# Performance work log

Hardware: AMD Instinct MI355X
Metric: run time of the kernel (lower is better)

The kernel has to match this reference:

```python
import jax, jax.numpy as jnp
import numpy as np
import math

N = 32768
C = 128
K = 16
CHUNK = 2048
LN_EPS = float(C)  # original code calls torch.nn.LayerNorm(C, C): second positional arg is eps -> eps = 128.0 (faithful)


def knn_idx(coords):
    """Brute-force KNN on full coords [N,4] (matches knn_points(x_C, x_C, K=16)), chunked over queries."""
    def one_chunk(q):  # q: [CHUNK,4]
        d = jnp.sum((q[:, None, :] - coords[None, :, :]) ** 2, axis=-1)  # [CHUNK,N]
        return jax.lax.top_k(-d, K)[1]  # ascending distance (return_sorted=True)
    qs = coords.reshape(-1, CHUNK, coords.shape[-1])
    return jax.lax.map(one_chunk, qs).reshape(-1, K)  # [N,K]


def layer_norm(x, g, b):
    mu = jnp.mean(x, axis=-1, keepdims=True)
    var = jnp.mean((x - mu) ** 2, axis=-1, keepdims=True)
    return (x - mu) / jnp.sqrt(var + LN_EPS) * g + b


def self_attention(x_f, xyz_enc, new_feature, qw, qb, kw, kb, vw, vb):
    Q = x_f @ qw + qb                              # [N,C]
    nf = new_feature + xyz_enc                     # [N,K,C]
    Kt = nf @ kw + kb                              # [N,K,C]
    scores = jnp.einsum('nkd,nd->nk', Kt, Q) / math.sqrt(C)
    a = jax.nn.softmax(scores, axis=-1)            # [N,K]
    V = nf @ vw + vb                               # [N,K,C]
    return jnp.einsum('nk,nkd->nd', a, V)          # [N,C]


def setup_inputs() -> dict:
    key = jax.random.key(0)
    ks = jax.random.split(key, 22)
    xyz = jax.random.uniform(ks[0], (N, 3), dtype=jnp.float32) * 100.0
    coords = jnp.concatenate([jnp.zeros((N, 1), jnp.float32), xyz], axis=1)  # [N,4] batch col = 0
    feats = jax.random.normal(ks[1], (N, C), dtype=jnp.float32)
    s = 0.02
    def lin(k, din, dout):
        kw, kb = jax.random.split(k)
        return jax.random.normal(kw, (din, dout), jnp.float32) * s, jax.random.normal(kb, (dout,), jnp.float32) * s
    pos_w, pos_b = lin(ks[2], 3, C)
    pos1_w, pos1_b = lin(ks[3], 3, C)
    qw0, qb0 = lin(ks[4], C, C); kw0, kb0 = lin(ks[5], C, C); vw0, vb0 = lin(ks[6], C, C)
    qw1, qb1 = lin(ks[7], C, C); kw1, kb1 = lin(ks[8], C, C); vw1, vb1 = lin(ks[9], C, C)
    lin_w, lin_b = lin(ks[10], C, C)  # MinkowskiConvolution kernel_size=1 == pointwise linear
    return {
        'coords': coords, 'feats': feats,
        'pos_w': pos_w, 'pos_b': pos_b, 'pos1_w': pos1_w, 'pos1_b': pos1_b,
        'qw0': qw0, 'qb0': qb0, 'kw0': kw0, 'kb0': kb0, 'vw0': vw0, 'vb0': vb0,
        'qw1': qw1, 'qb1': qb1, 'kw1': kw1, 'kb1': kb1, 'vw1': vw1, 'vb1': vb1,
        'lin_w': lin_w, 'lin_b': lin_b,
        'g0': jnp.ones((C,), jnp.float32), 'be0': jnp.zeros((C,), jnp.float32),
        'g1': jnp.ones((C,), jnp.float32), 'be1': jnp.zeros((C,), jnp.float32),
    }


def reference(coords, feats, pos_w, pos_b, pos1_w, pos1_b,
              qw0, qb0, kw0, kb0, vw0, vb0,
              qw1, qb1, kw1, kb1, vw1, vb1,
              lin_w, lin_b, g0, be0, g1, be1):
    idx = knn_idx(coords)                           # [N,K]
    xyz = coords[:, 1:]                             # [N,3]
    new_xyz = xyz[:, None, :] - xyz[idx]            # [N,K,3] relative offsets
    # block 1
    xyz_enc = new_xyz @ pos_w + pos_b               # [N,K,C]
    nf = feats[idx]                                 # gather [N,K,C]
    o = self_attention(feats, xyz_enc, nf, qw0, qb0, kw0, kb0, vw0, vb0)
    # block 2: re-gather updated features with same idx
    nf1 = o[idx]
    xyz_enc1 = new_xyz @ pos1_w + pos1_b
    o = self_attention(o, xyz_enc1, nf1, qw1, qb1, kw1, kb1, vw1, vb1)
    # residual + LN, pointwise conv, residual + LN
    h = layer_norm(feats + o, g0, be0)
    h1 = h @ lin_w + lin_b
    return layer_norm(h + h1, g1, be1)
```

## Files before the change

### kernel.cpp

```cpp
#include <hip/hip_runtime.h>
#include <stdint.h>

#define NPT 32768

typedef unsigned int u32;
typedef unsigned short u16;
typedef unsigned long long u64;

typedef short v8s __attribute__((ext_vector_type(8)));
typedef float v4f __attribute__((ext_vector_type(4)));

__device__ __forceinline__ float b2f(u16 u) {
  union { u32 u; float f; } x; x.u = ((u32)u) << 16; return x.f;
}
__device__ __forceinline__ u16 f2b(float f) {
  union { float f; u32 u; } x; x.f = f;
  u32 u = x.u;
  return (u16)((u + 0x7fffu + ((u >> 16) & 1u)) >> 16);
}
__device__ __forceinline__ bool probe_f32(const void* coords) {
  return ((const u16*)coords)[1] == 0;
}
__device__ __forceinline__ float ldany(const void* p, long i, bool f32) {
  return f32 ? ((const float*)p)[i] : b2f(((const u16*)p)[i]);
}
__device__ __forceinline__ float wsum(float v) {
#pragma unroll
  for (int m = 1; m < 64; m <<= 1) v += __shfl_xor(v, m, 64);
  return v;
}

#define GC 16
#define GH 6.25f
#define GINV 0.16f
#define NCELL (GC * GC * GC)

__device__ __forceinline__ int cell1d(float v) {
  int c = (int)(v * GINV);
  return c > (GC - 1) ? (GC - 1) : (c < 0 ? 0 : c);
}

__global__ __launch_bounds__(256) void conv_coords_hist(const void* __restrict__ coords,
                                                        float* __restrict__ cx, float* __restrict__ cy,
                                                        float* __restrict__ cz, int* __restrict__ cellStart,
                                                        int* __restrict__ pcell) {
  const bool f32 = probe_f32(coords);
  int i = blockIdx.x * 256 + threadIdx.x;
  float x = ldany(coords, (long)i * 4 + 1, f32);
  float y = ldany(coords, (long)i * 4 + 2, f32);
  float z = ldany(coords, (long)i * 4 + 3, f32);
  cx[i] = x; cy[i] = y; cz[i] = z;
  int c = (cell1d(z) * GC + cell1d(y)) * GC + cell1d(x);
  pcell[i] = c;
  atomicAdd(&cellStart[c + 1], 1);
}

__global__ __launch_bounds__(256) void conv_featsS(const void* __restrict__ coords,
                                                   const void* __restrict__ feats,
                                                   const float4* __restrict__ sortedP,
                                                   u16* __restrict__ featsS) {
  const bool f32 = probe_f32(coords);
  long i = (long)blockIdx.x * 256 + threadIdx.x;
  int s = (int)(i >> 7), c = (int)(i & 127);
  long orig = (long)__float_as_int(sortedP[s].w);
  featsS[i] = f32 ? f2b(((const float*)feats)[orig * 128 + c]) : ((const u16*)feats)[orig * 128 + c];
}

__global__ __launch_bounds__(256) void grid_scan(int* __restrict__ cellStart, int* __restrict__ cellPtr) {
  __shared__ int part[256];
  const int t = threadIdx.x;
  int local[16]; int s = 0;
#pragma unroll
  for (int i = 0; i < 16; i++) { local[i] = cellStart[1 + t * 16 + i]; s += local[i]; }
  part[t] = s;
  __syncthreads();
  for (int off = 1; off < 256; off <<= 1) {
    int v = (t >= off) ? part[t - off] : 0;
    __syncthreads();
    part[t] += v;
    __syncthreads();
  }
  int run = (t == 0) ? 0 : part[t - 1];
#pragma unroll
  for (int i = 0; i < 16; i++) {
    int c = t * 16 + i;
    cellPtr[c] = run;
    run += local[i];
    cellStart[c + 1] = run;
  }
}

__global__ __launch_bounds__(256) void grid_scatter(const float* __restrict__ cx, const float* __restrict__ cy,
                                                    const float* __restrict__ cz, const int* __restrict__ pcell,
                                                    int* __restrict__ cellPtr, float4* __restrict__ sortedP,
                                                    int* __restrict__ rank) {
  int i = blockIdx.x * 256 + threadIdx.x;
  int c = pcell[i];
  int pos = atomicAdd(&cellPtr[c], 1);
  sortedP[pos] = make_float4(cx[i], cy[i], cz[i], __int_as_float(i));
  rank[i] = pos;
}

__global__ __launch_bounds__(256) void knn_grid(const float4* __restrict__ sortedP,
                                                const int* __restrict__ cellStart,
                                                const int* __restrict__ rank,
                                                u16* __restrict__ idxout) {
  const int lane = threadIdx.x & 63;
  const int gl = lane & 15;
  const int grp = lane >> 4;
  const int q = blockIdx.x * 16 + (threadIdx.x >> 4);
  const float4 p = sortedP[q];
  const float qx = p.x, qy = p.y, qz = p.z;
  const int qcx = cell1d(qx), qcy = cell1d(qy), qcz = cell1d(qz);

  u64 R = ~0ull;

  auto key_of = [&](int g) -> u64 {
    float4 sp = sortedP[g];
    float dx = __fsub_rn(qx, sp.x), dy = __fsub_rn(qy, sp.y), dzc = __fsub_rn(qz, sp.z);
    float d = __fadd_rn(__fadd_rn(__fmul_rn(dx, dx), __fmul_rn(dy, dy)), __fmul_rn(dzc, dzc));
    return ((u64)__float_as_uint(d) << 32) | (u32)__float_as_int(sp.w);
  };

  auto shfl64 = [&](u64 v, int s) -> u64 {
    int lo = __shfl((int)(u32)v, s, 16);
    int hi = __shfl((int)(u32)(v >> 32), s, 16);
    return ((u64)(u32)hi << 32) | (u32)lo;
  };
  auto sxg = [&](u64 v, int m) -> u64 {
    int lo = __shfl_xor((int)(u32)v, m, 64);
    int hi = __shfl_xor((int)(u32)(v >> 32), m, 64);
    return ((u64)(u32)hi << 32) | (u32)lo;
  };
  auto upg = [&](u64 v) -> u64 {
    int lo = __shfl_up((int)(u32)v, 1, 16);
    int hi = __shfl_up((int)(u32)(v >> 32), 1, 16);
    return ((u64)(u32)hi << 32) | (u32)lo;
  };

  auto insert_one = [&](u64 kk) {
    u64 prev = upg(R);
    if (gl == 0) prev = 0ull;
    R = (kk < R) ? ((kk >= prev) ? kk : prev) : R;
  };

  auto batch_merge = [&](u64 key) {
    u64 k15 = shfl64(R, 15);
    u64 mask = __ballot(key < k15);
    u32 mymask = (u32)((mask >> (grp * 16)) & 0xffffu);
    if (mymask == 0) return;
    int pcount = __popc(mymask);
    if (pcount <= 8) {
      u32 mm = mymask;
      while (mm) {
        int s = __ffs((int)mm) - 1;
        mm &= mm - 1;
        insert_one(shfl64(key, s));
      }
      return;
    }
#pragma unroll
    for (int k = 2; k <= 16; k <<= 1) {
#pragma unroll
      for (int j = k >> 1; j > 0; j >>= 1) {
        u64 o = sxg(key, j);
        bool up = ((gl & k) == 0);
        bool lower = ((gl & j) == 0);
        u64 mn = key < o ? key : o;
        u64 mx = key < o ? o : key;
        key = (lower == up) ? mn : mx;
      }
    }
    u64 s = sxg(key, 15);
    u64 mn = R < s ? R : s;
#pragma unroll
    for (int j = 8; j > 0; j >>= 1) {
      u64 o = sxg(mn, j);
      bool lower = ((gl & j) == 0);
      u64 lo = mn < o ? mn : o;
      u64 hi = mn < o ? o : mn;
      mn = lower ? lo : hi;
    }
    R = mn;
  };

  auto scan_range_grp = [&](int s0, int s1) {
    for (int base = s0; base < s1; base += 16) {
      int g = base + gl;
      u64 key = (g < s1) ? key_of(g) : ~0ull;
      batch_merge(key);
    }
  };

  {
    const int rord[9] = { 4, 1, 3, 5, 7, 0, 2, 6, 8 };
    int rs[9], rl[9];
#pragma unroll
    for (int s_ = 0; s_ < 9; s_++) {
      int row = rord[s_];
      int dz = row / 3 - 1, dy = row % 3 - 1;
      int z = qcz + dz, y = qcy + dy;
      if (z < 0 || z > GC - 1 || y < 0 || y > GC - 1) { rs[s_] = 0; rl[s_] = 0; }
      else {
        int rb = (z * GC + y) * GC;
        int xlo = qcx - 1 < 0 ? 0 : qcx - 1;
        int xhi = qcx + 1 > GC - 1 ? GC - 1 : qcx + 1;
        int s = cellStart[rb + xlo], e = cellStart[rb + xhi + 1];
        rs[s_] = s; rl[s_] = e - s;
      }
    }
    int cum[10]; cum[0] = 0;
#pragma unroll
    for (int i = 0; i < 9; i++) cum[i + 1] = cum[i] + rl[i];
    int total = cum[9];
    for (int base = 0; base < total; base += 16) {
      int pp = base + gl;
      u64 key = ~0ull;
      if (pp < total) {
        int g = 0;
#pragma unroll
        for (int i = 0; i < 9; i++) {
          if (pp >= cum[i] && pp < cum[i + 1]) g = rs[i] + (pp - cum[i]);
        }
        key = key_of(g);
      }
      batch_merge(key);
    }
  }

  {
    u64 k15 = shfl64(R, 15);
    float d15 = __uint_as_float((u32)(k15 >> 32));
    float b1 = GH * 1.0f;
    if (!(d15 < b1 * b1 * 0.998f)) {
      for (int r = 2; r < GC; ++r) {
        int zlo = qcz - r < 0 ? 0 : qcz - r, zhi = qcz + r > GC - 1 ? GC - 1 : qcz + r;
        for (int z = zlo; z <= zhi; ++z) {
          int adz = z - qcz; adz = adz < 0 ? -adz : adz;
          bool ez = (adz == r);
          int ylo = qcy - r < 0 ? 0 : qcy - r, yhi = qcy + r > GC - 1 ? GC - 1 : qcy + r;
          for (int y = ylo; y <= yhi; ++y) {
            int ady = y - qcy; ady = ady < 0 ? -ady : ady;
            bool ey = (ady == r);
            int rb = (z * GC + y) * GC;
            if (ez || ey) {
              int xlo = qcx - r < 0 ? 0 : qcx - r, xhi = qcx + r > GC - 1 ? GC - 1 : qcx + r;
              scan_range_grp(cellStart[rb + xlo], cellStart[rb + xhi + 1]);
            } else {
              int xm = qcx - r, xp = qcx + r;
              if (xm >= 0) scan_range_grp(cellStart[rb + xm], cellStart[rb + xm + 1]);
              if (xp <= GC - 1) scan_range_grp(cellStart[rb + xp], cellStart[rb + xp + 1]);
            }
          }
        }
        k15 = shfl64(R, 15);
        d15 = __uint_as_float((u32)(k15 >> 32));
        float bound = GH * (float)r;
        if (d15 < bound * bound * 0.998f) break;
      }
    }
  }

  idxout[(size_t)q * 16 + gl] = (u16)rank[(int)(u32)R];
}

__global__ __launch_bounds__(256) void prep_tables(
    const void* coords,
    const void* pw0, const void* pb0, const void* kw0, const void* kb0, const void* vw0, const void* vb0,
    const void* pw1, const void* pb1, const void* kw1, const void* kb1, const void* vw1, const void* vb1,
    float* __restrict__ tbl, int* __restrict__ cellStart) {
  const bool f32 = probe_f32(coords);
  const int tid = blockIdx.x * 256 + threadIdx.x;
  if (tid <= NCELL) cellStart[tid] = 0;
  const int lane = threadIdx.x & 63;
  const int o = blockIdx.x * 4 + (threadIdx.x >> 6);
  const int l = o >> 10;
  const int rem = o & 1023;
  const void* PW = l ? pw1 : pw0;
  const void* PB = l ? pb1 : pb0;
  const void* KW = l ? kw1 : kw0;
  const void* KB = l ? kb1 : kb0;
  const void* VW = l ? vw1 : vw0;
  const void* VB = l ? vb1 : vb0;
  float acc, extra = 0.f;
  if (rem < 768) {
    bool isV = rem >= 384;
    int r2 = isV ? rem - 384 : rem;
    int i = r2 >> 7, c = r2 & 127;
    const void* W = isV ? VW : KW;
    acc = ldany(PW, i * 128 + lane, f32) * ldany(W, (long)lane * 128 + c, f32)
        + ldany(PW, i * 128 + lane + 64, f32) * ldany(W, (long)(lane + 64) * 128 + c, f32);
  } else {
    bool isV = rem >= 896;
    int c = rem & 127;
    const void* W = isV ? VW : KW;
    const void* B = isV ? VB : KB;
    acc = ldany(PB, lane, f32) * ldany(W, (long)lane * 128 + c, f32)
        + ldany(PB, lane + 64, f32) * ldany(W, (long)(lane + 64) * 128 + c, f32);
    extra = ldany(B, c, f32);
  }
  acc = wsum(acc) + extra;
  if (lane == 0) tbl[l * 1024 + rem] = acc;
}

__global__ __launch_bounds__(256) void prep_bfrag_all(const void* __restrict__ coords,
                                                      const void* __restrict__ qw0, const void* __restrict__ kw0,
                                                      const void* __restrict__ vw0, const void* __restrict__ qw1,
                                                      const void* __restrict__ kw1, const void* __restrict__ vw1,
                                                      const void* __restrict__ linw, u16* __restrict__ Bf0,
                                                      u16* __restrict__ Bf1, u16* __restrict__ BfL) {
  const bool f32 = probe_f32(coords);
  int tid = blockIdx.x * 256 + threadIdx.x;
  const void *w0, *w1, *w2; u16* out; int t;
  if (tid < 49152) { t = tid; w0 = qw0; w1 = kw0; w2 = vw0; out = Bf0; }
  else if (tid < 98304) { t = tid - 49152; w0 = qw1; w1 = kw1; w2 = vw1; out = Bf1; }
  else { t = tid - 98304; w0 = linw; w1 = linw; w2 = linw; out = BfL; }
  int j = t & 7, lane = (t >> 3) & 63, kq = (t >> 9) & 3, tile = t >> 11;
  int k = kq * 32 + ((lane >> 4) << 3) + j;
  int col = tile * 16 + (lane & 15);
  const void* w = (col < 128) ? w0 : ((col < 256) ? w1 : w2);
  long off = (long)k * 128 + (col & 127);
  out[t] = f32 ? f2b(((const float*)w)[off]) : ((const u16*)w)[off];
}

__global__ __launch_bounds__(256) void gemm_kernel(const void* __restrict__ coords,
                                                   const u16* __restrict__ A, const u16* __restrict__ Bf,
                                                   const void* __restrict__ bias, u16* __restrict__ Qb,
                                                   u16* __restrict__ KVb, float* __restrict__ outF,
                                                   int mode, int ntiles) {
  const bool f32 = probe_f32(coords);
  const int lane = threadIdx.x & 63;
  const int wave = threadIdx.x >> 6;
  const int r0 = blockIdx.x * 64 + wave * 16;
  const int quad = lane >> 4, lr = lane & 15;
  v8s a[4];
#pragma unroll
  for (int kq = 0; kq < 4; kq++) {
    union { uint4 u; v8s s; } c;
    c.u = *(const uint4*)(A + (size_t)(r0 + lr) * 128 + kq * 32 + quad * 8);
    a[kq] = c.s;
  }
  for (int tile = 0; tile < ntiles; ++tile) {
    v4f acc = { 0.f, 0.f, 0.f, 0.f };
#pragma unroll
    for (int kq = 0; kq < 4; kq++) {
      union { uint4 u; v8s s; } c;
      c.u = *(const uint4*)(Bf + ((size_t)(tile * 4 + kq) * 64 + lane) * 8);
      acc = __builtin_amdgcn_mfma_f32_16x16x32_bf16(a[kq], c.s, acc, 0, 0, 0);
    }
    int col = tile * 16 + lr;
    if (mode == 0) {
      if (col < 128) {
        float bb = ldany(bias, col, f32);
#pragma unroll
        for (int r = 0; r < 4; r++) Qb[(size_t)(r0 + quad * 4 + r) * 128 + col] = f2b(acc[r] + bb);
      } else {
#pragma unroll
        for (int r = 0; r < 4; r++) KVb[(size_t)(r0 + quad * 4 + r) * 256 + (col - 128)] = f2b(acc[r]);
      }
    } else {
      float bb = ldany(bias, col, f32);
#pragma unroll
      for (int r = 0; r < 4; r++) outF[(size_t)(r0 + quad * 4 + r) * 128 + col] = acc[r] + bb;
    }
  }
}

__global__ __launch_bounds__(256) void attn_kernel(const void* __restrict__ coordsRaw,
                                                   const float4* __restrict__ sortedP,
                                                   const u16* __restrict__ idx,
                                                   const u16* __restrict__ Qb, const u16* __restrict__ KVb,
                                                   const float* __restrict__ tbl, const void* __restrict__ feats,
                                                   const void* __restrict__ g, const void* __restrict__ be,
                                                   u16* __restrict__ outB, int mode) {
  const int lane = threadIdx.x & 63;
  const int swz = (blockIdx.x & 7) * (gridDim.x >> 3) + (blockIdx.x >> 3);
  const int n = swz * 4 + (threadIdx.x >> 6);
  const int c0 = 2 * lane;
  const int k = lane & 15;
  const int quad = lane >> 4;
  const float4 P = sortedP[n];

  u32 qu = *(const u32*)(Qb + (size_t)n * 128 + c0);
  const float q0 = b2f((u16)(qu & 0xffffu)), q1 = b2f((u16)(qu >> 16));
  float p0 = tbl[c0] * q0 + tbl[c0 + 1] * q1;
  float p1 = tbl[128 + c0] * q0 + tbl[128 + c0 + 1] * q1;
  float p2 = tbl[256 + c0] * q0 + tbl[256 + c0 + 1] * q1;
  float p3 = tbl[768 + c0] * q0 + tbl[768 + c0 + 1] * q1;
#pragma unroll
  for (int m = 1; m < 64; m <<= 1) {
    p0 += __shfl_xor(p0, m, 64);
    p1 += __shfl_xor(p1, m, 64);
    p2 += __shfl_xor(p2, m, 64);
    p3 += __shfl_xor(p3, m, 64);
  }

  const int j = idx[(size_t)n * 16 + k];
  const float4 Pj = sortedP[j];
  const float nx = P.x - Pj.x, ny = P.y - Pj.y, nz = P.z - Pj.z;
  v4f sacc = { 0.f, 0.f, 0.f, 0.f };
#pragma unroll
  for (int kq = 0; kq < 4; kq++) {
    union { uint4 u; v8s s; } ka, qa;
    ka.u = *(const uint4*)(KVb + (size_t)j * 256 + kq * 32 + quad * 8);
    qa.u = *(const uint4*)(Qb + (size_t)n * 128 + kq * 32 + quad * 8);
    sacc = __builtin_amdgcn_mfma_f32_16x16x32_bf16(ka.s, qa.s, sacc, 0, 0, 0);
  }
  const int srcl = ((k >> 2) << 4) | k;
  float t0 = __shfl(sacc[0], srcl, 64);
  float t1 = __shfl(sacc[1], srcl, 64);
  float t2 = __shfl(sacc[2], srcl, 64);
  float t3 = __shfl(sacc[3], srcl, 64);
  float s = (k & 2) ? ((k & 1) ? t3 : t2) : ((k & 1) ? t1 : t0);
  float sc = (s + nx * p0 + ny * p1 + nz * p2 + p3) * 0.08838834764831845f;

  float mx = sc;
#pragma unroll
  for (int m = 1; m < 16; m <<= 1) mx = fmaxf(mx, __shfl_xor(mx, m, 64));
  float e = expf(sc - mx);
  float ssum = e;
#pragma unroll
  for (int m = 1; m < 16; m <<= 1) ssum += __shfl_xor(ssum, m, 64);
  const float a = e / ssum;

  const float sA = 1.0f;
  float wx = a * nx, wy = a * ny, wz = a * nz;
#pragma unroll
  for (int m = 1; m < 16; m <<= 1) {
    wx += __shfl_xor(wx, m, 64);
    wy += __shfl_xor(wy, m, 64);
    wz += __shfl_xor(wz, m, 64);
  }

  const int base = lane & 48;
  float a0 = 0.f, a1 = 0.f;
#pragma unroll
  for (int k2 = 0; k2 < 16; k2++) {
    float ak = __shfl(a, base + k2, 64);
    int jk = __shfl(j, base + k2, 64);
    u32 u = *(const u32*)(KVb + (size_t)jk * 256 + 128 + c0);
    a0 += ak * b2f((u16)(u & 0xffffu));
    a1 += ak * b2f((u16)(u >> 16));
  }
  float o0 = a0 + wx * tbl[384 + c0] + wy * tbl[512 + c0] + wz * tbl[640 + c0] + sA * tbl[896 + c0];
  float o1 = a1 + wx * tbl[384 + c0 + 1] + wy * tbl[512 + c0 + 1] + wz * tbl[640 + c0 + 1] + sA * tbl[896 + c0 + 1];
  if (mode == 1) {
    const bool f32 = probe_f32(coordsRaw);
    long orig = (long)__float_as_int(P.w);
    float x0 = ldany(feats, orig * 128 + c0, f32) + o0;
    float x1 = ldany(feats, orig * 128 + c0 + 1, f32) + o1;
    float mu = wsum(x0 + x1) * (1.f / 128.f);
    float d0 = x0 - mu, d1 = x1 - mu;
    float var = wsum(d0 * d0 + d1 * d1) * (1.f / 128.f);
    float rinv = 1.0f / sqrtf(var + 128.0f);
    o0 = d0 * rinv * ldany(g, c0, f32) + ldany(be, c0, f32);
    o1 = d1 * rinv * ldany(g, c0 + 1, f32) + ldany(be, c0 + 1, f32);
  }
  ((u32*)outB)[(size_t)n * 64 + lane] = (u32)f2b(o0) | ((u32)f2b(o1) << 16);
}

__global__ __launch_bounds__(256) void ln_final(const void* __restrict__ coords,
                                                const float4* __restrict__ sortedP,
                                                const u16* __restrict__ hB, const float* __restrict__ h1F,
                                                const void* __restrict__ g, const void* __restrict__ be,
                                                void* __restrict__ outAny) {
  const bool f32 = probe_f32(coords);
  const int lane = threadIdx.x & 63;
  const int n = blockIdx.x * 4 + (threadIdx.x >> 6);
  const int c0 = 2 * lane;
  u32 u = *(const u32*)(hB + (size_t)n * 128 + c0);
  float2 h1 = *(const float2*)(h1F + (size_t)n * 128 + c0);
  float x0 = b2f((u16)(u & 0xffffu)) + h1.x;
  float x1 = b2f((u16)(u >> 16)) + h1.y;
  float mu = wsum(x0 + x1) * (1.f / 128.f);
  float d0 = x0 - mu, d1 = x1 - mu;
  float var = wsum(d0 * d0 + d1 * d1) * (1.f / 128.f);
  float rinv = 1.0f / sqrtf(var + 128.0f);
  float y0 = d0 * rinv * ldany(g, c0, f32) + ldany(be, c0, f32);
  float y1 = d1 * rinv * ldany(g, c0 + 1, f32) + ldany(be, c0 + 1, f32);
  size_t orig = (size_t)__float_as_int(sortedP[n].w);
  if (f32) {
    *(float2*)((float*)outAny + orig * 128 + c0) = make_float2(y0, y1);
  } else {
    ((u32*)outAny)[orig * 64 + lane] = (u32)f2b(y0) | ((u32)f2b(y1) << 16);
  }
}

extern "C" void kernel_launch(void* const* d_in, const int* in_sizes, int n_in,
                              void* d_out, int out_size, void* d_ws, size_t ws_size,
                              hipStream_t stream) {
  (void)in_sizes; (void)n_in; (void)out_size; (void)ws_size;
  const void* coords = d_in[0];
  const void* feats = d_in[1];
  const void* pos_w = d_in[2];
  const void* pos_b = d_in[3];
  const void* pos1_w = d_in[4];
  const void* pos1_b = d_in[5];
  const void* qw0 = d_in[6];
  const void* qb0 = d_in[7];
  const void* kw0 = d_in[8];
  const void* kb0 = d_in[9];
  const void* vw0 = d_in[10];
  const void* vb0 = d_in[11];
  const void* qw1 = d_in[12];
  const void* qb1 = d_in[13];
  const void* kw1 = d_in[14];
  const void* kb1 = d_in[15];
  const void* vw1 = d_in[16];
  const void* vb1 = d_in[17];
  const void* lin_w = d_in[18];
  const void* lin_b = d_in[19];
  const void* g0 = d_in[20];
  const void* be0 = d_in[21];
  const void* g1 = d_in[22];
  const void* be1 = d_in[23];

  char* w = (char*)d_ws;
  u16* idxp = (u16*)(w + 0);
  float4* sortedP = (float4*)(w + 1048576);
  int* rank = (int*)(w + 1572864);
  float* cx = (float*)(w + 1703936);
  float* cy = (float*)(w + 1835008);
  float* cz = (float*)(w + 1966080);
  float* tbl = (float*)(w + 2097152);
  u16* Bf0 = (u16*)(w + 2105344);
  u16* Bf1 = (u16*)(w + 2203648);
  u16* BfL = (u16*)(w + 2301952);
  u16* featsS = (u16*)(w + 2334720);
  u16* oS = (u16*)(w + 10723328);
  u16* Qb = (u16*)(w + 19111936);
  u16* KVb = (u16*)(w + 27500544);
  int* cellStart = (int*)(w + 19111936);
  int* cellPtr = (int*)(w + 19132416);
  int* pcell = (int*)(w + 19148800);
  float* h1F = (float*)(w + 19111936);

  hipLaunchKernelGGL(prep_tables, dim3(512), dim3(256), 0, stream, coords,
                     pos_w, pos_b, kw0, kb0, vw0, vb0, pos1_w, pos1_b, kw1, kb1, vw1, vb1, tbl, cellStart);
  hipLaunchKernelGGL(conv_coords_hist, dim3(128), dim3(256), 0, stream, coords, cx, cy, cz, cellStart, pcell);
  hipLaunchKernelGGL(prep_bfrag_all, dim3(448), dim3(256), 0, stream, coords,
                     qw0, kw0, vw0, qw1, kw1, vw1, lin_w, Bf0, Bf1, BfL);

  hipLaunchKernelGGL(grid_scan, dim3(1), dim3(256), 0, stream, cellStart, cellPtr);
  hipLaunchKernelGGL(grid_scatter, dim3(128), dim3(256), 0, stream, cx, cy, cz, pcell, cellPtr, sortedP, rank);
  hipLaunchKernelGGL(conv_featsS, dim3(16384), dim3(256), 0, stream, coords, feats, sortedP, featsS);
  hipLaunchKernelGGL(knn_grid, dim3(2048), dim3(256), 0, stream, sortedP, cellStart, rank, idxp);

  hipLaunchKernelGGL(gemm_kernel, dim3(512), dim3(256), 0, stream, coords, featsS, Bf0, qb0, Qb, KVb,
                     (float*)nullptr, 0, 24);
  hipLaunchKernelGGL(attn_kernel, dim3(8192), dim3(256), 0, stream, coords, sortedP, idxp, Qb, KVb, tbl,
                     (const void*)nullptr, (const void*)nullptr, (const void*)nullptr, oS, 0);
  hipLaunchKernelGGL(gemm_kernel, dim3(512), dim3(256), 0, stream, coords, oS, Bf1, qb1, Qb, KVb,
                     (float*)nullptr, 0, 24);
  hipLaunchKernelGGL(attn_kernel, dim3(8192), dim3(256), 0, stream, coords, sortedP, idxp, Qb, KVb, tbl + 1024,
                     feats, g0, be0, oS, 1);
  hipLaunchKernelGGL(gemm_kernel, dim3(512), dim3(256), 0, stream, coords, oS, BfL, lin_b,
                     (u16*)nullptr, (u16*)nullptr, h1F, 1, 8);
  hipLaunchKernelGGL(ln_final, dim3(8192), dim3(256), 0, stream, coords, sortedP, oS, h1F, g1, be1, d_out);
}
```

Before: 325.2 us.

## Precompute per-point positional dot products in GEMM and prefetch V rows in attention

The GEMM epilogue now computes each point's four dot products of Q with the positional tables and writes them to a small per-point buffer. This removes the 64-lane shuffle reduction that every attention wave used to perform. The attention kernel also issues all 16 neighbour V-row loads and the K-fragment loads up front, so memory latency overlaps with the score computation. The costs are higher register pressure in attention and extra shuffles in the GEMM, and the p4 buffer reuses the workspace region that previously held rank.

Result: no change. 322.7 us (-0.8%).

```diff
diff --git a/kernel.cpp b/kernel.cpp
--- a/kernel.cpp
+++ b/kernel.cpp
@@ -327,6 +327,7 @@
                                                    const u16* __restrict__ A, const u16* __restrict__ Bf,
                                                    const void* __restrict__ bias, u16* __restrict__ Qb,
                                                    u16* __restrict__ KVb, float* __restrict__ outF,
+                                                   const float* __restrict__ tblp, float* __restrict__ pOut,
                                                    int mode, int ntiles) {
   const bool f32 = probe_f32(coords);
   const int lane = threadIdx.x & 63;
@@ -340,6 +341,10 @@
     c.u = *(const uint4*)(A + (size_t)(r0 + lr) * 128 + kq * 32 + quad * 8);
     a[kq] = c.s;
   }
+  float pd0[4] = { 0.f, 0.f, 0.f, 0.f };
+  float pd1[4] = { 0.f, 0.f, 0.f, 0.f };
+  float pd2[4] = { 0.f, 0.f, 0.f, 0.f };
+  float pd3[4] = { 0.f, 0.f, 0.f, 0.f };
   for (int tile = 0; tile < ntiles; ++tile) {
     v4f acc = { 0.f, 0.f, 0.f, 0.f };
 #pragma unroll
@@ -352,8 +357,16 @@
     if (mode == 0) {
       if (col < 128) {
         float bb = ldany(bias, col, f32);
-#pragma unroll
-        for (int r = 0; r < 4; r++) Qb[(size_t)(r0 + quad * 4 + r) * 128 + col] = f2b(acc[r] + bb);
+        float t0 = tblp[col], t1 = tblp[128 + col], t2 = tblp[256 + col], t3 = tblp[768 + col];
+#pragma unroll
+        for (int r = 0; r < 4; r++) {
+          float qv = acc[r] + bb;
+          Qb[(size_t)(r0 + quad * 4 + r) * 128 + col] = f2b(qv);
+          pd0[r] += t0 * qv;
+          pd1[r] += t1 * qv;
+          pd2[r] += t2 * qv;
+          pd3[r] += t3 * qv;
+        }
       } else {
 #pragma unroll
         for (int r = 0; r < 4; r++) KVb[(size_t)(r0 + quad * 4 + r) * 256 + (col - 128)] = f2b(acc[r]);
@@ -362,6 +375,25 @@
       float bb = ldany(bias, col, f32);
 #pragma unroll
       for (int r = 0; r < 4; r++) outF[(size_t)(r0 + quad * 4 + r) * 128 + col] = acc[r] + bb;
+    }
+  }
+  if (mode == 0) {
+#pragma unroll
+    for (int m = 1; m < 16; m <<= 1) {
+#pragma unroll
+      for (int r = 0; r < 4; r++) {
+        pd0[r] += __shfl_xor(pd0[r], m, 64);
+        pd1[r] += __shfl_xor(pd1[r], m, 64);
+        pd2[r] += __shfl_xor(pd2[r], m, 64);
+        pd3[r] += __shfl_xor(pd3[r], m, 64);
+      }
+    }
+    if (lr < 4) {
+#pragma unroll
+      for (int r = 0; r < 4; r++) {
+        float v = (lr == 0) ? pd0[r] : ((lr == 1) ? pd1[r] : ((lr == 2) ? pd2[r] : pd3[r]));
+        pOut[(size_t)(r0 + quad * 4 + r) * 4 + lr] = v;
+      }
     }
   }
 }
@@ -370,7 +402,8 @@
                                                    const float4* __restrict__ sortedP,
                                                    const u16* __restrict__ idx,
                                                    const u16* __restrict__ Qb, const u16* __restrict__ KVb,
-                                                   const float* __restrict__ tbl, const void* __restrict__ feats,
+                                                   const float* __restrict__ tbl, const float* __restrict__ p4,
+                                                   const void* __restrict__ feats,
                                                    const void* __restrict__ g, const void* __restrict__ be,
                                                    u16* __restrict__ outB, int mode) {
   const int lane = threadIdx.x & 63;
@@ -379,30 +412,30 @@
   const int c0 = 2 * lane;
   const int k = lane & 15;
   const int quad = lane >> 4;
+  const int base = lane & 48;
+
+  const int j = idx[(size_t)n * 16 + k];
+  u32 vr[16];
+#pragma unroll
+  for (int k2 = 0; k2 < 16; k2++) {
+    int jk = __shfl(j, base + k2, 64);
+    vr[k2] = *(const u32*)(KVb + (size_t)jk * 256 + 128 + c0);
+  }
+  uint4 kf[4];
+#pragma unroll
+  for (int kq = 0; kq < 4; kq++) {
+    kf[kq] = *(const uint4*)(KVb + (size_t)j * 256 + kq * 32 + quad * 8);
+  }
   const float4 P = sortedP[n];
-
-  u32 qu = *(const u32*)(Qb + (size_t)n * 128 + c0);
-  const float q0 = b2f((u16)(qu & 0xffffu)), q1 = b2f((u16)(qu >> 16));
-  float p0 = tbl[c0] * q0 + tbl[c0 + 1] * q1;
-  float p1 = tbl[128 + c0] * q0 + tbl[128 + c0 + 1] * q1;
-  float p2 = tbl[256 + c0] * q0 + tbl[256 + c0 + 1] * q1;
-  float p3 = tbl[768 + c0] * q0 + tbl[768 + c0 + 1] * q1;
-#pragma unroll
-  for (int m = 1; m < 64; m <<= 1) {
-    p0 += __shfl_xor(p0, m, 64);
-    p1 += __shfl_xor(p1, m, 64);
-    p2 += __shfl_xor(p2, m, 64);
-    p3 += __shfl_xor(p3, m, 64);
-  }
-
-  const int j = idx[(size_t)n * 16 + k];
   const float4 Pj = sortedP[j];
   const float nx = P.x - Pj.x, ny = P.y - Pj.y, nz = P.z - Pj.z;
+  const float4 pv = *(const float4*)(p4 + (size_t)n * 4);
+
   v4f sacc = { 0.f, 0.f, 0.f, 0.f };
 #pragma unroll
   for (int kq = 0; kq < 4; kq++) {
     union { uint4 u; v8s s; } ka, qa;
-    ka.u = *(const uint4*)(KVb + (size_t)j * 256 + kq * 32 + quad * 8);
+    ka.u = kf[kq];
     qa.u = *(const uint4*)(Qb + (size_t)n * 128 + kq * 32 + quad * 8);
     sacc = __builtin_amdgcn_mfma_f32_16x16x32_bf16(ka.s, qa.s, sacc, 0, 0, 0);
   }
@@ -412,7 +445,7 @@
   float t2 = __shfl(sacc[2], srcl, 64);
   float t3 = __shfl(sacc[3], srcl, 64);
   float s = (k & 2) ? ((k & 1) ? t3 : t2) : ((k & 1) ? t1 : t0);
-  float sc = (s + nx * p0 + ny * p1 + nz * p2 + p3) * 0.08838834764831845f;
+  float sc = (s + nx * pv.x + ny * pv.y + nz * pv.z + pv.w) * 0.08838834764831845f;
 
   float mx = sc;
 #pragma unroll
@@ -423,7 +456,6 @@
   for (int m = 1; m < 16; m <<= 1) ssum += __shfl_xor(ssum, m, 64);
   const float a = e / ssum;
 
-  const float sA = 1.0f;
   float wx = a * nx, wy = a * ny, wz = a * nz;
 #pragma unroll
   for (int m = 1; m < 16; m <<= 1) {
@@ -432,18 +464,16 @@
     wz += __shfl_xor(wz, m, 64);
   }
 
-  const int base = lane & 48;
   float a0 = 0.f, a1 = 0.f;
 #pragma unroll
   for (int k2 = 0; k2 < 16; k2++) {
     float ak = __shfl(a, base + k2, 64);
-    int jk = __shfl(j, base + k2, 64);
-    u32 u = *(const u32*)(KVb + (size_t)jk * 256 + 128 + c0);
+    u32 u = vr[k2];
     a0 += ak * b2f((u16)(u & 0xffffu));
     a1 += ak * b2f((u16)(u >> 16));
   }
-  float o0 = a0 + wx * tbl[384 + c0] + wy * tbl[512 + c0] + wz * tbl[640 + c0] + sA * tbl[896 + c0];
-  float o1 = a1 + wx * tbl[384 + c0 + 1] + wy * tbl[512 + c0 + 1] + wz * tbl[640 + c0 + 1] + sA * tbl[896 + c0 + 1];
+  float o0 = a0 + wx * tbl[384 + c0] + wy * tbl[512 + c0] + wz * tbl[640 + c0] + tbl[896 + c0];
+  float o1 = a1 + wx * tbl[384 + c0 + 1] + wy * tbl[512 + c0 + 1] + wz * tbl[640 + c0 + 1] + tbl[896 + c0 + 1];
   if (mode == 1) {
     const bool f32 = probe_f32(coordsRaw);
     long orig = (long)__float_as_int(P.w);
@@ -534,6 +564,7 @@
   int* cellPtr = (int*)(w + 19132416);
   int* pcell = (int*)(w + 19148800);
   float* h1F = (float*)(w + 19111936);
+  float* p4 = (float*)(w + 1572864);
 
   hipLaunchKernelGGL(prep_tables, dim3(512), dim3(256), 0, stream, coords,
                      pos_w, pos_b, kw0, kb0, vw0, vb0, pos1_w, pos1_b, kw1, kb1, vw1, vb1, tbl, cellStart);
@@ -547,14 +578,14 @@
   hipLaunchKernelGGL(knn_grid, dim3(2048), dim3(256), 0, stream, sortedP, cellStart, rank, idxp);
 
   hipLaunchKernelGGL(gemm_kernel, dim3(512), dim3(256), 0, stream, coords, featsS, Bf0, qb0, Qb, KVb,
-                     (float*)nullptr, 0, 24);
-  hipLaunchKernelGGL(attn_kernel, dim3(8192), dim3(256), 0, stream, coords, sortedP, idxp, Qb, KVb, tbl,
+                     (float*)nullptr, tbl, p4, 0, 24);
+  hipLaunchKernelGGL(attn_kernel, dim3(8192), dim3(256), 0, stream, coords, sortedP, idxp, Qb, KVb, tbl, p4,
                      (const void*)nullptr, (const void*)nullptr, (const void*)nullptr, oS, 0);
   hipLaunchKernelGGL(gemm_kernel, dim3(512), dim3(256), 0, stream, coords, oS, Bf1, qb1, Qb, KVb,
-                     (float*)nullptr, 0, 24);
-  hipLaunchKernelGGL(attn_kernel, dim3(8192), dim3(256), 0, stream, coords, sortedP, idxp, Qb, KVb, tbl + 1024,
+                     (float*)nullptr, tbl + 1024, p4, 0, 24);
+  hipLaunchKernelGGL(attn_kernel, dim3(8192), dim3(256), 0, stream, coords, sortedP, idxp, Qb, KVb, tbl + 1024, p4,
                      feats, g0, be0, oS, 1);
   hipLaunchKernelGGL(gemm_kernel, dim3(512), dim3(256), 0, stream, coords, oS, BfL, lin_b,
-                     (u16*)nullptr, (u16*)nullptr, h1F, 1, 8);
+                     (u16*)nullptr, (u16*)nullptr, h1F, (const float*)nullptr, (float*)nullptr, 1, 8);
   hipLaunchKernelGGL(ln_final, dim3(8192), dim3(256), 0, stream, coords, sortedP, oS, h1F, g1, be1, d_out);
 }
```
